# Kernel optimization log

Hardware: AMD Instinct MI355X
Metric: run time of the kernel (lower is better)

The kernel has to match this reference:

```python
import jax, jax.numpy as jnp
import numpy as np

H = 8
SPLIT = 1
# deterministic stand-in for random.shuffle(range(8)) in the original
_PERM = np.random.RandomState(0).permutation(H)
SERIES_IDX = jnp.asarray(_PERM[SPLIT:])  # 7 heads
CROSS_IDX = jnp.asarray(_PERM[:SPLIT])   # 1 head


def setup_inputs() -> dict:
    key = jax.random.key(0)
    ks = jax.random.split(key, 5)
    B, L, E = 8, 1024, 64
    shp = (B, L, H, E)
    return {
        "queries": jax.random.normal(ks[0], shp, dtype=jnp.float32),
        "keys": jax.random.normal(ks[1], shp, dtype=jnp.float32),
        "keysT": jax.random.normal(ks[2], shp, dtype=jnp.float32),
        "values": jax.random.normal(ks[3], shp, dtype=jnp.float32),
        "valuesT": jax.random.normal(ks[4], shp, dtype=jnp.float32),
    }


def reference(queries, keys, keysT, values, valuesT):
    B, L, _, E = queries.shape
    scale = 1.0 / jnp.sqrt(jnp.asarray(E, dtype=queries.dtype))
    neg_inf = jnp.asarray(-jnp.inf, dtype=queries.dtype)

    # head split (gather along head dim)
    sq = queries[:, :, SERIES_IDX]   # [B,L,7,E]
    sk = keys[:, :, SERIES_IDX]      # [B,S,7,E]
    sv = values[:, :, SERIES_IDX]    # [B,S,7,D]
    cq = queries[:, :, CROSS_IDX]    # [B,L,1,E]
    ckT = keysT[:, :, CROSS_IDX]     # [B,C,1,E]
    cvT = valuesT[:, :, CROSS_IDX]   # [B,C,1,D]

    # causal mask: True above the diagonal -> disallowed
    causal = jnp.triu(jnp.ones((L, L), dtype=bool), k=1)  # [L,L]

    # series branch
    scores = jnp.einsum('blne,bsne->bnls', sq, sk)  # [B,7,L,S]
    scores = jnp.where(causal[None, None], neg_inf, scores * scale)
    series = jax.nn.softmax(scores, axis=-1)
    V = jnp.einsum('bhls,bshd->blhd', series, sv)   # [B,L,7,D]

    # cross branch
    cscores = jnp.einsum('blme,bcme->bmlc', cq, ckT)  # [B,1,L,C]
    cscores = jnp.where(causal[None, None], neg_inf, cscores * scale)
    crosses = jax.nn.softmax(cscores, axis=-1)
    V_cross = jnp.einsum('bhlc,bchd->blhd', crosses, cvT)  # [B,L,1,D]

    return jnp.concatenate([V, V_cross], axis=2)  # [B,L,8,D]
```

## Files before the change

kernel.cpp:

```cpp
#include <hip/hip_runtime.h>
#include <math.h>

#define Lq 1024
#define Hq 8
#define Eq 64
#define LDW 72
#define PTW 40

#define SRC_HEAD_PACKED 0x64503712u

typedef __bf16 bf16_t;
typedef __bf16 bf16x8 __attribute__((ext_vector_type(8)));
typedef __bf16 bf16x4 __attribute__((ext_vector_type(4)));
typedef float floatx4 __attribute__((ext_vector_type(4)));

__device__ __forceinline__ bf16x8 cvt8(const float4 a, const float4 b) {
    bf16x8 r;
    r[0] = (bf16_t)a.x; r[1] = (bf16_t)a.y; r[2] = (bf16_t)a.z; r[3] = (bf16_t)a.w;
    r[4] = (bf16_t)b.x; r[5] = (bf16_t)b.y; r[6] = (bf16_t)b.z; r[7] = (bf16_t)b.w;
    return r;
}

__global__ __launch_bounds__(512, 4)
void attn_mfma(const float* __restrict__ Q, const float* __restrict__ Ks,
               const float* __restrict__ KTs, const float* __restrict__ Vs,
               const float* __restrict__ VTs, float* __restrict__ out) {
    const int slot = blockIdx.x;
    const int b    = blockIdx.y;
    const int qt   = 15 - blockIdx.z;
    const int h    = (SRC_HEAD_PACKED >> (slot * 4)) & 0xF;
    const float* __restrict__ Kp = (slot == 7) ? KTs : Ks;
    const float* __restrict__ Vp = (slot == 7) ? VTs : Vs;

    const int tid  = threadIdx.x;
    const int wv   = tid >> 6;
    const int lane = tid & 63;
    const int ln16 = lane & 15;
    const int quad = lane >> 4;
    const int wq   = wv & 3;
    const int kh   = wv >> 2;

    __shared__ alignas(16) unsigned short smem[64 * LDW * 2 + 8 * 16 * PTW];
    unsigned short (*k_lds)[LDW]  = (unsigned short (*)[LDW])smem;
    unsigned short (*vt_lds)[LDW] = (unsigned short (*)[LDW])(smem + 64 * LDW);
    unsigned short (*pt)[PTW]     = (unsigned short (*)[PTW])(smem + 2 * 64 * LDW + wv * 16 * PTW);

    const float qs = 0.125f * 1.44269504f;
    bf16x8 qf[2];
    {
        const int r = qt * 64 + wq * 16 + ln16;
        const float* qa = Q + (((size_t)b * Lq + r) * Hq + h) * Eq + quad * 8;
        #pragma unroll
        for (int ec = 0; ec < 2; ++ec) {
            float4 f0 = ((const float4*)(qa + ec * 32))[0];
            float4 f1 = ((const float4*)(qa + ec * 32))[1];
            f0.x*=qs; f0.y*=qs; f0.z*=qs; f0.w*=qs;
            f1.x*=qs; f1.y*=qs; f1.z*=qs; f1.w*=qs;
            qf[ec] = cvt8(f0, f1);
        }
    }

    floatx4 O[4];
    #pragma unroll
    for (int i = 0; i < 4; ++i) O[i] = (floatx4){0, 0, 0, 0};
    float m = -1e30f, l = 0.f;

    float4 kq[2];
    float  vq[8];
    const int kj = tid >> 3, kc = (tid & 7) * 8;
    const int vd = tid & 63, vk = wv * 8;

    auto load_tile = [&](int kt) {
        const float* kb = Kp + (((size_t)b * Lq + kt * 64 + kj) * Hq + h) * Eq + kc;
        kq[0] = ((const float4*)kb)[0]; kq[1] = ((const float4*)kb)[1];
        const float* vb = Vp + (((size_t)b * Lq + kt * 64 + vk) * Hq + h) * Eq + vd;
        #pragma unroll
        for (int i = 0; i < 8; ++i) vq[i] = vb[(size_t)i * (Hq * Eq)];
    };

    load_tile(0);
    for (int kt = 0; kt <= qt; ++kt) {
        __syncthreads();
        *(bf16x8*)&k_lds[kj][kc] = cvt8(kq[0], kq[1]);
        {
            const float4* vq4 = (const float4*)vq;
            *(bf16x8*)&vt_lds[vd][vk] = cvt8(vq4[0], vq4[1]);
        }
        if (kt < qt) load_tile(kt + 1);
        __syncthreads();

        bf16x8 kf[2][2], vf[4];
        #pragma unroll
        for (int c = 0; c < 2; ++c) {
            kf[c][0] = *(const bf16x8*)&k_lds[(kh * 2 + c) * 16 + ln16][quad * 8];
            kf[c][1] = *(const bf16x8*)&k_lds[(kh * 2 + c) * 16 + ln16][32 + quad * 8];
        }
        #pragma unroll
        for (int c = 0; c < 4; ++c)
            vf[c] = *(const bf16x8*)&vt_lds[c * 16 + ln16][kh * 32 + quad * 8];

        floatx4 s[2];
        #pragma unroll
        for (int nc = 0; nc < 2; ++nc) {
            floatx4 acc = (floatx4){0, 0, 0, 0};
            acc = __builtin_amdgcn_mfma_f32_16x16x32_bf16(kf[nc][0], qf[0], acc, 0, 0, 0);
            acc = __builtin_amdgcn_mfma_f32_16x16x32_bf16(kf[nc][1], qf[1], acc, 0, 0, 0);
            s[nc] = acc;
        }
        if (kt == qt) {
            const int rin = wq * 16 + ln16;
            #pragma unroll
            for (int nc = 0; nc < 2; ++nc)
                #pragma unroll
                for (int r = 0; r < 4; ++r)
                    if (kh * 32 + nc * 16 + quad * 4 + r > rin) s[nc][r] = -INFINITY;
        }
        float mn = s[0][0];
        #pragma unroll
        for (int nc = 0; nc < 2; ++nc)
            #pragma unroll
            for (int r = 0; r < 4; ++r) mn = fmaxf(mn, s[nc][r]);
        mn = fmaxf(mn, __shfl_xor(mn, 16, 64));
        mn = fmaxf(mn, __shfl_xor(mn, 32, 64));
        mn = fmaxf(mn, m);
        const float alpha = __builtin_amdgcn_exp2f(m - mn);
        m = mn;
        float ps = 0.f;
        float pv[2][4];
        #pragma unroll
        for (int nc = 0; nc < 2; ++nc)
            #pragma unroll
            for (int r = 0; r < 4; ++r) {
                pv[nc][r] = __builtin_amdgcn_exp2f(s[nc][r] - mn);
                ps += pv[nc][r];
            }
        ps += __shfl_xor(ps, 16, 64);
        ps += __shfl_xor(ps, 32, 64);
        l = l * alpha + ps;
        #pragma unroll
        for (int dc = 0; dc < 4; ++dc) O[dc] *= alpha;
        #pragma unroll
        for (int nc = 0; nc < 2; ++nc) {
            bf16x4 pk;
            pk[0] = (bf16_t)pv[nc][0]; pk[1] = (bf16_t)pv[nc][1];
            pk[2] = (bf16_t)pv[nc][2]; pk[3] = (bf16_t)pv[nc][3];
            *(bf16x4*)&pt[ln16][nc * 16 + quad * 4] = pk;
        }
        bf16x8 pf = *(const bf16x8*)&pt[ln16][quad * 8];
        #pragma unroll
        for (int dc = 0; dc < 4; ++dc)
            O[dc] = __builtin_amdgcn_mfma_f32_16x16x32_bf16(vf[dc], pf, O[dc], 0, 0, 0);
    }

    __syncthreads();
    float* mb = (float*)smem;
    if (kh) {
        float* dst = mb + (wq * 64 + lane) * 18;
        #pragma unroll
        for (int dc = 0; dc < 4; ++dc) {
            *(float2*)(dst + dc * 4)     = make_float2(O[dc][0], O[dc][1]);
            *(float2*)(dst + dc * 4 + 2) = make_float2(O[dc][2], O[dc][3]);
        }
        dst[16] = m; dst[17] = l;
    }
    __syncthreads();
    if (!kh) {
        const float* src = mb + (wq * 64 + lane) * 18;
        const float m1 = src[16], l1 = src[17];
        const float mm = fmaxf(m, m1);
        const float a0 = __builtin_amdgcn_exp2f(m - mm);
        const float a1 = __builtin_amdgcn_exp2f(m1 - mm);
        const float inv = 1.0f / (l * a0 + l1 * a1);
        const int row = qt * 64 + wq * 16 + ln16;
        float* op = out + (((size_t)b * Lq + row) * Hq + slot) * Eq + quad * 4;
        #pragma unroll
        for (int dc = 0; dc < 4; ++dc) {
            float4 o;
            o.x = (O[dc][0] * a0 + src[dc * 4 + 0] * a1) * inv;
            o.y = (O[dc][1] * a0 + src[dc * 4 + 1] * a1) * inv;
            o.z = (O[dc][2] * a0 + src[dc * 4 + 2] * a1) * inv;
            o.w = (O[dc][3] * a0 + src[dc * 4 + 3] * a1) * inv;
            *(float4*)(op + dc * 16) = o;
        }
    }
}

extern "C" void kernel_launch(void* const* d_in, const int* in_sizes, int n_in,
                              void* d_out, int out_size, void* d_ws, size_t ws_size,
                              hipStream_t stream) {
    const float* queries = (const float*)d_in[0];
    const float* keys    = (const float*)d_in[1];
    const float* keysT   = (const float*)d_in[2];
    const float* values  = (const float*)d_in[3];
    const float* valuesT = (const float*)d_in[4];
    float* out = (float*)d_out;

    dim3 grid(Hq, 8, 16);
    dim3 block(512);
    attn_mfma<<<grid, block, 0, stream>>>(queries, keys, keysT, values, valuesT, out);
}
```

Measured before the change: 132.5 us.

## Double-buffer K/V tiles in LDS and feed P to MFMA from registers

K/V tiles are now staged into two alternating LDS buffers with a global prefetch two tiles ahead. This cuts the loop to one barrier per iteration and lets staging overlap compute. When the 16x16x16 bf16 MFMA builtin exists, the P matrix goes straight from registers into MFMA instead of round-tripping through per-wave LDS scratch. The cost is double the MFMA instruction count for PV, more LDS, and a custom barrier with inline waitcnt.

Result: no change. 134.0 us (+1.1%).

```diff
diff --git a/kernel.cpp b/kernel.cpp
--- a/kernel.cpp
+++ b/kernel.cpp
@@ -6,12 +6,21 @@
 #define Eq 64
 #define LDW 72
 #define PTW 40
+#define KV_SH (64 * LDW)
+#define BUF_SH (2 * KV_SH)
 
 #define SRC_HEAD_PACKED 0x64503712u
+
+#if __has_builtin(__builtin_amdgcn_mfma_f32_16x16x16bf16_1k)
+#define HAVE_MFMA16 1
+#else
+#define HAVE_MFMA16 0
+#endif
 
 typedef __bf16 bf16_t;
 typedef __bf16 bf16x8 __attribute__((ext_vector_type(8)));
 typedef __bf16 bf16x4 __attribute__((ext_vector_type(4)));
+typedef short short4v __attribute__((ext_vector_type(4)));
 typedef float floatx4 __attribute__((ext_vector_type(4)));
 
 __device__ __forceinline__ bf16x8 cvt8(const float4 a, const float4 b) {
@@ -19,6 +28,12 @@
     r[0] = (bf16_t)a.x; r[1] = (bf16_t)a.y; r[2] = (bf16_t)a.z; r[3] = (bf16_t)a.w;
     r[4] = (bf16_t)b.x; r[5] = (bf16_t)b.y; r[6] = (bf16_t)b.z; r[7] = (bf16_t)b.w;
     return r;
+}
+
+__device__ __forceinline__ void block_sync_lds() {
+    asm volatile("s_waitcnt lgkmcnt(0)" ::: "memory");
+    __builtin_amdgcn_s_barrier();
+    __builtin_amdgcn_sched_barrier(0);
 }
 
 __global__ __launch_bounds__(512, 4)
@@ -40,10 +55,10 @@
     const int wq   = wv & 3;
     const int kh   = wv >> 2;
 
-    __shared__ alignas(16) unsigned short smem[64 * LDW * 2 + 8 * 16 * PTW];
-    unsigned short (*k_lds)[LDW]  = (unsigned short (*)[LDW])smem;
-    unsigned short (*vt_lds)[LDW] = (unsigned short (*)[LDW])(smem + 64 * LDW);
-    unsigned short (*pt)[PTW]     = (unsigned short (*)[PTW])(smem + 2 * 64 * LDW + wv * 16 * PTW);
+    __shared__ alignas(16) unsigned short smem[2 * BUF_SH + (1 - HAVE_MFMA16) * 8 * 16 * PTW];
+#if !HAVE_MFMA16
+    unsigned short (*pt)[PTW] = (unsigned short (*)[PTW])(smem + 2 * BUF_SH + wv * 16 * PTW);
+#endif
 
     const float qs = 0.125f * 1.44269504f;
     bf16x8 qf[2];
@@ -77,27 +92,29 @@
         #pragma unroll
         for (int i = 0; i < 8; ++i) vq[i] = vb[(size_t)i * (Hq * Eq)];
     };
+    auto stage = [&](int bsel) {
+        unsigned short* dst = smem + bsel * BUF_SH;
+        *(bf16x8*)&dst[kj * LDW + kc] = cvt8(kq[0], kq[1]);
+        const float4* vq4 = (const float4*)vq;
+        *(bf16x8*)&dst[KV_SH + vd * LDW + vk] = cvt8(vq4[0], vq4[1]);
+    };
 
     load_tile(0);
+    stage(0);
+    load_tile(1);
+    block_sync_lds();
+
     for (int kt = 0; kt <= qt; ++kt) {
-        __syncthreads();
-        *(bf16x8*)&k_lds[kj][kc] = cvt8(kq[0], kq[1]);
-        {
-            const float4* vq4 = (const float4*)vq;
-            *(bf16x8*)&vt_lds[vd][vk] = cvt8(vq4[0], vq4[1]);
-        }
-        if (kt < qt) load_tile(kt + 1);
-        __syncthreads();
-
-        bf16x8 kf[2][2], vf[4];
+        const unsigned short* base = smem + (kt & 1) * BUF_SH;
+
+        bf16x8 kf[2][2];
         #pragma unroll
         for (int c = 0; c < 2; ++c) {
-            kf[c][0] = *(const bf16x8*)&k_lds[(kh * 2 + c) * 16 + ln16][quad * 8];
-            kf[c][1] = *(const bf16x8*)&k_lds[(kh * 2 + c) * 16 + ln16][32 + quad * 8];
-        }
-        #pragma unroll
-        for (int c = 0; c < 4; ++c)
-            vf[c] = *(const bf16x8*)&vt_lds[c * 16 + ln16][kh * 32 + quad * 8];
+            kf[c][0] = *(const bf16x8*)&base[((kh * 2 + c) * 16 + ln16) * LDW + quad * 8];
+            kf[c][1] = *(const bf16x8*)&base[((kh * 2 + c) * 16 + ln16) * LDW + 32 + quad * 8];
+        }
+        if (kt < qt) stage((kt + 1) & 1);
+        if (kt + 1 < qt) load_tile(kt + 2);
 
         floatx4 s[2];
         #pragma unroll
@@ -107,6 +124,21 @@
             acc = __builtin_amdgcn_mfma_f32_16x16x32_bf16(kf[nc][1], qf[1], acc, 0, 0, 0);
             s[nc] = acc;
         }
+
+#if HAVE_MFMA16
+        bf16x4 va[4][2];
+        #pragma unroll
+        for (int dc = 0; dc < 4; ++dc)
+            #pragma unroll
+            for (int nc = 0; nc < 2; ++nc)
+                va[dc][nc] = *(const bf16x4*)&base[KV_SH + (dc * 16 + ln16) * LDW + kh * 32 + nc * 16 + quad * 4];
+#else
+        bf16x8 vf[4];
+        #pragma unroll
+        for (int c = 0; c < 4; ++c)
+            vf[c] = *(const bf16x8*)&base[KV_SH + (c * 16 + ln16) * LDW + kh * 32 + quad * 8];
+#endif
+
         if (kt == qt) {
             const int rin = wq * 16 + ln16;
             #pragma unroll
@@ -139,6 +171,23 @@
         l = l * alpha + ps;
         #pragma unroll
         for (int dc = 0; dc < 4; ++dc) O[dc] *= alpha;
+
+#if HAVE_MFMA16
+        short4v pb[2];
+        #pragma unroll
+        for (int nc = 0; nc < 2; ++nc) {
+            bf16x4 t;
+            t[0] = (bf16_t)pv[nc][0]; t[1] = (bf16_t)pv[nc][1];
+            t[2] = (bf16_t)pv[nc][2]; t[3] = (bf16_t)pv[nc][3];
+            pb[nc] = __builtin_bit_cast(short4v, t);
+        }
+        #pragma unroll
+        for (int dc = 0; dc < 4; ++dc)
+            #pragma unroll
+            for (int nc = 0; nc < 2; ++nc)
+                O[dc] = __builtin_amdgcn_mfma_f32_16x16x16bf16_1k(
+                    __builtin_bit_cast(short4v, va[dc][nc]), pb[nc], O[dc], 0, 0, 0);
+#else
         #pragma unroll
         for (int nc = 0; nc < 2; ++nc) {
             bf16x4 pk;
@@ -150,9 +199,11 @@
         #pragma unroll
         for (int dc = 0; dc < 4; ++dc)
             O[dc] = __builtin_amdgcn_mfma_f32_16x16x32_bf16(vf[dc], pf, O[dc], 0, 0, 0);
-    }
-
-    __syncthreads();
+#endif
+
+        block_sync_lds();
+    }
+
     float* mb = (float*)smem;
     if (kh) {
         float* dst = mb + (wq * 64 + lane) * 18;
```
